# Kernel tuning notes

Hardware: AMD Instinct MI355X
Metric: run time of the kernel (lower is better)

The kernel has to match this reference:

```python
import jax, jax.numpy as jnp
import numpy as np

REG_WEIGHT = 1e-4
N_LAYERS = 3


def setup_inputs() -> dict:
    key = jax.random.key(0)
    ks = jax.random.split(key, 7)
    n_users, n_items, d = 100000, 50000, 64
    E, B = 1600000, 4096
    return {
        "user_table": jax.random.normal(ks[0], (n_users, d), dtype=jnp.float32) * 0.01,
        "item_table": jax.random.normal(ks[1], (n_items, d), dtype=jnp.float32) * 0.01,
        "edge_u": jax.random.randint(ks[2], (E,), 0, n_users, dtype=jnp.int32),
        "edge_i": jax.random.randint(ks[3], (E,), 0, n_items, dtype=jnp.int32),
        "users": jax.random.randint(ks[4], (B,), 0, n_users, dtype=jnp.int32),
        "pos_items": jax.random.randint(ks[5], (B,), 0, n_items, dtype=jnp.int32),
        "neg_items": jax.random.randint(ks[6], (B,), 0, n_items, dtype=jnp.int32),
    }


def _lightgcn_embeddings(user_table, item_table, edge_u, edge_i):
    n_users, n_items = user_table.shape[0], item_table.shape[0]
    N = n_users + n_items
    E = edge_u.shape[0]
    ones = jnp.ones((E,), dtype=user_table.dtype)
    # symmetric normalization D^{-1/2} A D^{-1/2} on the bipartite graph
    deg_u = jax.ops.segment_sum(ones, edge_u, num_segments=n_users)
    deg_i = jax.ops.segment_sum(ones, edge_i, num_segments=n_items)
    w = jax.lax.rsqrt(jnp.maximum(deg_u[edge_u] * deg_i[edge_i], 1.0))
    # symmetric edge list over the stacked [users; items] node set
    rows = jnp.concatenate([edge_u, edge_i + n_users])
    cols = jnp.concatenate([edge_i + n_users, edge_u])
    vals = jnp.concatenate([w, w])[:, None]

    x = jnp.concatenate([user_table, item_table], axis=0)  # [N, d]
    acc = x
    for _ in range(N_LAYERS):
        x = jax.ops.segment_sum(x[cols] * vals, rows, num_segments=N)
        acc = acc + x
    final = acc / jnp.asarray(N_LAYERS + 1, dtype=x.dtype)
    return final[:n_users], final[n_users:]


def reference(user_table, item_table, edge_u, edge_i, users, pos_items, neg_items):
    user_emb_all, item_emb_all = _lightgcn_embeddings(user_table, item_table, edge_u, edge_i)
    u_emb = user_emb_all[users]
    pos_i_emb = item_emb_all[pos_items]
    neg_i_emb = item_emb_all[neg_items]
    pos_scores = jnp.sum(u_emb * pos_i_emb, axis=-1)
    neg_scores = jnp.sum(u_emb * neg_i_emb, axis=-1)
    # L2 regularization on the layer-0 (table) embeddings
    u0 = user_table[users]
    p0 = item_table[pos_items]
    n0 = item_table[neg_items]
    reg_loss = REG_WEIGHT * (jnp.sum(u0 * u0) + jnp.sum(p0 * p0) + jnp.sum(n0 * n0))
    reg_loss = reg_loss / users.shape[0]
    return pos_scores, neg_scores, reg_loss
```

## Files before the change

### kernel.cpp

```cpp
#include <hip/hip_runtime.h>
#include <hip/hip_fp16.h>

#define THREADS 256
#define BIN_C2 4096
#define NBMAX 392
#define CAP 4608
#define SH_U 8
#define SH_I 7
#define CPAD 16
#define T_TILES 8
#define TSH_U 13
#define TSH_I 14

__global__ void binpack(const int* __restrict__ eu, const int* __restrict__ ei,
                        int* __restrict__ regu, int* __restrict__ regi,
                        int* __restrict__ sTu, int* __restrict__ sTi,
                        int E, int nbu, int nbi) {
    int c = blockIdx.x;
    bool isU = (blockIdx.y == 0);
    const int* key   = isU ? eu : ei;
    const int* other = isU ? ei : eu;
    int nb   = isU ? nbu : nbi;
    int sh   = isU ? SH_U : SH_I;
    int losh = isU ? 16 : 17;
    int lomsk = (1 << sh) - 1;
    int* reg = isU ? regu : regi;
    int* sT  = (isU ? sTu : sTi) + (size_t)c * (NBMAX);
    __shared__ int hist[NBMAX];
    __shared__ int wsum[4];
    int tid = threadIdx.x;
    int e0 = c * BIN_C2;
    int cnt = min(BIN_C2, E - e0);
    if (cnt <= 0) return;
    for (int b = tid; b < nb; b += THREADS) hist[b] = 0;
    __syncthreads();
    for (int k = tid; k < cnt; k += THREADS)
        atomicAdd(&hist[key[e0 + k] >> sh], 1);
    __syncthreads();
    int b0 = tid * 2;
    int v0 = (b0 < nb)     ? hist[b0]     : 0;
    int v1 = (b0 + 1 < nb) ? hist[b0 + 1] : 0;
    int s2 = v0 + v1;
    int lane = tid & 63, wid = tid >> 6;
    int inc = s2;
    #pragma unroll
    for (int ofs = 1; ofs < 64; ofs <<= 1) {
        int t = __shfl_up(inc, ofs);
        if (lane >= ofs) inc += t;
    }
    if (lane == 63) wsum[wid] = inc;
    __syncthreads();
    int wofs = 0;
    #pragma unroll
    for (int w = 0; w < 4; ++w) wofs += (w < wid) ? wsum[w] : 0;
    int excl = inc - s2 + wofs;
    __syncthreads();
    if (b0 < nb)     { hist[b0] = excl;          sT[b0] = excl; }
    if (b0 + 1 < nb) { hist[b0 + 1] = excl + v0; sT[b0 + 1] = excl + v0; }
    if (tid == THREADS - 1) sT[nb] = cnt;
    __syncthreads();
    for (int k = tid; k < cnt; k += THREADS) {
        int kn = key[e0 + k];
        int o  = other[e0 + k];
        int b  = kn >> sh;
        int p  = ((kn & lomsk) << losh) | o;
        int pos = atomicAdd(&hist[b], 1);
        reg[(size_t)c * BIN_C2 + pos] = p;
    }
}

__global__ void place(const int* __restrict__ regu, const int* __restrict__ regi,
                      const int* __restrict__ sTu, const int* __restrict__ sTi,
                      int* __restrict__ offu, int* __restrict__ offi,
                      int* __restrict__ du, int* __restrict__ di,
                      float* __restrict__ rsdu, float* __restrict__ rsdi,
                      int* __restrict__ entu, int* __restrict__ enti,
                      int* __restrict__ curs,
                      int nbu, int nU, int nI, int nchunks) {
    __shared__ int stash[CAP];
    __shared__ int bin_cnt[THREADS * T_TILES];
    __shared__ int node_base[THREADS];
    __shared__ int wsum[4];
    __shared__ int bob_sh;
    __shared__ int scursor;
    int b = blockIdx.x;
    bool isU = (b < nbu);
    int bidx = isU ? b : (b - nbu);
    const int* reg = isU ? regu : regi;
    const int* sT  = isU ? sTu : sTi;
    int base_node, nn;
    int *off, *deg, *ent; float* rsd;
    int losh, tsh;
    if (isU) {
        base_node = bidx << SH_U; nn = min(256, nU - base_node);
        off = offu; deg = du; rsd = rsdu; ent = entu;
        losh = 16; tsh = TSH_U;
    } else {
        base_node = bidx << SH_I; nn = min(128, nI - base_node);
        off = offi; deg = di; rsd = rsdi; ent = enti;
        losh = 17; tsh = TSH_I;
    }
    int lomask = (1 << losh) - 1;
    int tid = threadIdx.x;
    if (tid == 0) scursor = 0;
    #pragma unroll
    for (int t = 0; t < T_TILES; ++t) bin_cnt[tid + t * THREADS] = 0;
    __syncthreads();
    for (int c = tid; c < nchunks; c += THREADS) {
        const int* row = sT + (size_t)c * NBMAX;
        int s = row[bidx], e = row[bidx + 1];
        int len = e - s;
        if (len > 0) {
            int base = atomicAdd(&scursor, len);
            const int* src = reg + (size_t)c * BIN_C2 + s;
            for (int j = 0; j < len; ++j) {
                int pos = base + j;
                if (pos < CAP) stash[pos] = src[j];
            }
        }
    }
    __syncthreads();
    int count = min(scursor, CAP);
    for (int k = tid; k < count; k += THREADS) {
        int p = stash[k];
        int key = ((p >> losh) << 3) | ((p & lomask) >> tsh);
        atomicAdd(&bin_cnt[key], 1);
    }
    __syncthreads();
    int c = 0;
    {
        int base = tid * T_TILES;
        #pragma unroll
        for (int t = 0; t < T_TILES; ++t) {
            int v = bin_cnt[base + t];
            bin_cnt[base + t] = c;
            c += v;
        }
    }
    int seg = (c + 15) & ~15;
    int lane = tid & 63, wid = tid >> 6;
    int inc = seg;
    #pragma unroll
    for (int ofs = 1; ofs < 64; ofs <<= 1) {
        int t = __shfl_up(inc, ofs);
        if (lane >= ofs) inc += t;
    }
    if (lane == 63) wsum[wid] = inc;
    __syncthreads();
    int wofs = 0;
    #pragma unroll
    for (int w = 0; w < 4; ++w) wofs += (w < wid) ? wsum[w] : 0;
    int incl = inc + wofs;
    int excl = incl - seg;
    if (tid == THREADS - 1) bob_sh = atomicAdd(&curs[isU ? 0 : CPAD], incl);
    __syncthreads();
    int bob = bob_sh;
    node_base[tid] = excl;
    if (tid < nn) {
        off[base_node + tid] = bob + excl;
        deg[base_node + tid] = c;
        rsd[base_node + tid] = rsqrtf(fmaxf((float)c, 1.0f));
    }
    __syncthreads();
    #pragma unroll
    for (int t = 0; t < T_TILES; ++t) {
        int k = tid + t * THREADS;
        bin_cnt[k] += node_base[k >> 3];
    }
    __syncthreads();
    for (int k = tid; k < count; k += THREADS) {
        int p = stash[k];
        int key = ((p >> losh) << 3) | ((p & lomask) >> tsh);
        int sl = atomicAdd(&bin_cnt[key], 1);
        ent[bob + sl] = p & lomask;
    }
}

__global__ void conv16all(const float* __restrict__ ut, const float* __restrict__ it,
                          __half* __restrict__ dst, int nU16, int ntot16) {
    int stride = gridDim.x * blockDim.x;
    for (int i = blockIdx.x * blockDim.x + threadIdx.x; i < ntot16; i += stride) {
        const float* src = (i < nU16) ? (ut + (size_t)i * 4) : (it + (size_t)(i - nU16) * 4);
        float4 v = *reinterpret_cast<const float4*>(src);
        __half2 h0 = __float22half2_rn(make_float2(v.x, v.y));
        __half2 h1 = __float22half2_rn(make_float2(v.z, v.w));
        uint2 st;
        st.x = *reinterpret_cast<unsigned*>(&h0);
        st.y = *reinterpret_cast<unsigned*>(&h1);
        *reinterpret_cast<uint2*>(dst + (size_t)i * 4) = st;
    }
}

__global__ void prop16(const __half* __restrict__ x,
                       const int* __restrict__ offu, const int* __restrict__ offi,
                       const int* __restrict__ du, const int* __restrict__ di,
                       const float* __restrict__ rsdu, const float* __restrict__ rsdi,
                       const int* __restrict__ entu, const int* __restrict__ enti,
                       __half* __restrict__ y, int nU, int N) {
    int node = blockIdx.x * (THREADS >> 3) + (threadIdx.x >> 3);
    int lane = threadIdx.x & 7;
    if (node >= N) return;
    const int* ent; const __half* src; const float* rsdn;
    int beg, dg; float rs;
    if (node < nU) {
        beg = offu[node]; dg = du[node]; rs = rsdu[node];
        ent = entu; src = x + ((size_t)nU << 6); rsdn = rsdi;
    } else {
        int i = node - nU;
        beg = offi[i]; dg = di[i]; rs = rsdi[i];
        ent = enti; src = x; rsdn = rsdu;
    }
    float a0=0,a1=0,a2=0,a3=0,a4=0,a5=0,a6=0,a7=0;
    for (int k0 = 0; k0 < dg; k0 += 8) {
        int me = (k0 + lane < dg) ? ent[beg + k0 + lane] : 0;
        #pragma unroll
        for (int j = 0; j < 8; ++j) {
            if (k0 + j < dg) {
                int nbr = __shfl(me, j, 8);
                float w = rsdn[nbr];
                uint4 r = *reinterpret_cast<const uint4*>(src + ((size_t)nbr << 6) + (lane << 3));
                __half2 h0 = *reinterpret_cast<__half2*>(&r.x);
                __half2 h1 = *reinterpret_cast<__half2*>(&r.y);
                __half2 h2 = *reinterpret_cast<__half2*>(&r.z);
                __half2 h3 = *reinterpret_cast<__half2*>(&r.w);
                float2 f0 = __half22float2(h0), f1 = __half22float2(h1);
                float2 f2 = __half22float2(h2), f3 = __half22float2(h3);
                a0 += w * f0.x; a1 += w * f0.y; a2 += w * f1.x; a3 += w * f1.y;
                a4 += w * f2.x; a5 += w * f2.y; a6 += w * f3.x; a7 += w * f3.y;
            }
        }
    }
    __half2 o0 = __float22half2_rn(make_float2(a0 * rs, a1 * rs));
    __half2 o1 = __float22half2_rn(make_float2(a2 * rs, a3 * rs));
    __half2 o2 = __float22half2_rn(make_float2(a4 * rs, a5 * rs));
    __half2 o3 = __float22half2_rn(make_float2(a6 * rs, a7 * rs));
    uint4 st;
    st.x = *reinterpret_cast<unsigned*>(&o0);
    st.y = *reinterpret_cast<unsigned*>(&o1);
    st.z = *reinterpret_cast<unsigned*>(&o2);
    st.w = *reinterpret_cast<unsigned*>(&o3);
    *reinterpret_cast<uint4*>(y + ((size_t)node << 6) + (lane << 3)) = st;
}

__global__ void prop_sel_acc(const __half* __restrict__ x,
                             const int* __restrict__ users, const int* __restrict__ pos,
                             const int* __restrict__ neg,
                             const int* __restrict__ offu, const int* __restrict__ offi,
                             const int* __restrict__ du, const int* __restrict__ di,
                             const float* __restrict__ rsdu, const float* __restrict__ rsdi,
                             const int* __restrict__ entu, const int* __restrict__ enti,
                             float* __restrict__ sel, int B, int nU) {
    int r = blockIdx.x * (THREADS >> 3) + (threadIdx.x >> 3);
    int lane = threadIdx.x & 7;
    if (r >= 3 * B) return;
    int which = r / B, b = r - which * B;
    const int* ent; const __half* src; const float* rsdn;
    int beg, dg; float rs; size_t selfrow;
    if (which == 0) {
        int u = users[b];
        beg = offu[u]; dg = du[u]; rs = rsdu[u];
        ent = entu; src = x + ((size_t)nU << 6); rsdn = rsdi;
        selfrow = (size_t)u << 6;
    } else {
        int i = (which == 1) ? pos[b] : neg[b];
        beg = offi[i]; dg = di[i]; rs = rsdi[i];
        ent = enti; src = x; rsdn = rsdu;
        selfrow = (size_t)(nU + i) << 6;
    }
    float a0=0,a1=0,a2=0,a3=0,a4=0,a5=0,a6=0,a7=0;
    for (int k0 = 0; k0 < dg; k0 += 8) {
        int me = (k0 + lane < dg) ? ent[beg + k0 + lane] : 0;
        #pragma unroll
        for (int j = 0; j < 8; ++j) {
            if (k0 + j < dg) {
                int nbr = __shfl(me, j, 8);
                float w = rsdn[nbr];
                uint4 rv = *reinterpret_cast<const uint4*>(src + ((size_t)nbr << 6) + (lane << 3));
                __half2 h0 = *reinterpret_cast<__half2*>(&rv.x);
                __half2 h1 = *reinterpret_cast<__half2*>(&rv.y);
                __half2 h2 = *reinterpret_cast<__half2*>(&rv.z);
                __half2 h3 = *reinterpret_cast<__half2*>(&rv.w);
                float2 f0 = __half22float2(h0), f1 = __half22float2(h1);
                float2 f2 = __half22float2(h2), f3 = __half22float2(h3);
                a0 += w * f0.x; a1 += w * f0.y; a2 += w * f1.x; a3 += w * f1.y;
                a4 += w * f2.x; a5 += w * f2.y; a6 += w * f3.x; a7 += w * f3.y;
            }
        }
    }
    uint4 rv = *reinterpret_cast<const uint4*>(x + selfrow + (lane << 3));
    __half2 h0 = *reinterpret_cast<__half2*>(&rv.x);
    __half2 h1 = *reinterpret_cast<__half2*>(&rv.y);
    __half2 h2 = *reinterpret_cast<__half2*>(&rv.z);
    __half2 h3 = *reinterpret_cast<__half2*>(&rv.w);
    float2 s0 = __half22float2(h0), s1 = __half22float2(h1);
    float2 s2 = __half22float2(h2), s3 = __half22float2(h3);
    float* s = sel + ((size_t)r << 6) + (lane << 3);
    float4 d0 = *reinterpret_cast<float4*>(s);
    float4 d1 = *reinterpret_cast<float4*>(s + 4);
    d0.x += s0.x + rs * a0; d0.y += s0.y + rs * a1;
    d0.z += s1.x + rs * a2; d0.w += s1.y + rs * a3;
    d1.x += s2.x + rs * a4; d1.y += s2.y + rs * a5;
    d1.z += s3.x + rs * a6; d1.w += s3.y + rs * a7;
    *reinterpret_cast<float4*>(s) = d0;
    *reinterpret_cast<float4*>(s + 4) = d1;
}

__global__ void selreg(const float* __restrict__ ut, const float* __restrict__ it,
                       const int* __restrict__ users, const int* __restrict__ pos,
                       const int* __restrict__ neg,
                       float* __restrict__ sel, float* __restrict__ out_reg,
                       int B, float scale) {
    int r = blockIdx.x * (THREADS >> 4) + (threadIdx.x >> 4);
    int t = threadIdx.x & 15;
    float ssq = 0.f;
    if (r < 3 * B) {
        int which = r / B, b = r - which * B;
        const float* base; int idx;
        if (which == 0)      { base = ut; idx = users[b]; }
        else if (which == 1) { base = it; idx = pos[b]; }
        else                 { base = it; idx = neg[b]; }
        float4 v = *reinterpret_cast<const float4*>(base + ((size_t)idx << 6) + t * 4);
        *reinterpret_cast<float4*>(sel + ((size_t)r << 6) + t * 4) = v;
        ssq = v.x * v.x + v.y * v.y + v.z * v.z + v.w * v.w;
    }
    #pragma unroll
    for (int ofs = 32; ofs; ofs >>= 1) ssq += __shfl_down(ssq, ofs);
    if ((threadIdx.x & 63) == 0) atomicAdd(out_reg, ssq * scale);
}

__global__ void sel_acc16(const __half* __restrict__ x,
                          const int* __restrict__ users, const int* __restrict__ pos,
                          const int* __restrict__ neg, float* __restrict__ sel, int B, int nU) {
    int r = blockIdx.x * (THREADS >> 3) + (threadIdx.x >> 3);
    int lane = threadIdx.x & 7;
    if (r >= 3 * B) return;
    int which = r / B, b = r - which * B;
    size_t row;
    if (which == 0)      row = (size_t)users[b];
    else if (which == 1) row = (size_t)nU + pos[b];
    else                 row = (size_t)nU + neg[b];
    uint4 rv = *reinterpret_cast<const uint4*>(x + (row << 6) + (lane << 3));
    __half2 h0 = *reinterpret_cast<__half2*>(&rv.x);
    __half2 h1 = *reinterpret_cast<__half2*>(&rv.y);
    __half2 h2 = *reinterpret_cast<__half2*>(&rv.z);
    __half2 h3 = *reinterpret_cast<__half2*>(&rv.w);
    float2 f0 = __half22float2(h0), f1 = __half22float2(h1);
    float2 f2 = __half22float2(h2), f3 = __half22float2(h3);
    float* s = sel + ((size_t)r << 6) + (lane << 3);
    float4 d0 = *reinterpret_cast<float4*>(s);
    float4 d1 = *reinterpret_cast<float4*>(s + 4);
    d0.x += f0.x; d0.y += f0.y; d0.z += f1.x; d0.w += f1.y;
    d1.x += f2.x; d1.y += f2.y; d1.z += f3.x; d1.w += f3.y;
    *reinterpret_cast<float4*>(s) = d0;
    *reinterpret_cast<float4*>(s + 4) = d1;
}

__global__ void score(const float* __restrict__ sel, float* __restrict__ out, int B) {
    int b = blockIdx.x * (THREADS >> 6) + (threadIdx.x >> 6);
    int lane = threadIdx.x & 63;
    if (b >= B) return;
    float u = sel[((size_t)b << 6) + lane];
    float p = sel[((size_t)(B + b) << 6) + lane];
    float n = sel[((size_t)(2 * B + b) << 6) + lane];
    float ps = u * p, ns = u * n;
    for (int ofs = 32; ofs; ofs >>= 1) {
        ps += __shfl_down(ps, ofs);
        ns += __shfl_down(ns, ofs);
    }
    if (lane == 0) {
        out[b]     = ps * (1.0f / 16.0f);
        out[B + b] = ns * (1.0f / 16.0f);
    }
}

extern "C" void kernel_launch(void* const* d_in, const int* in_sizes, int n_in,
                              void* d_out, int out_size, void* d_ws, size_t ws_size,
                              hipStream_t stream) {
    const float* ut   = (const float*)d_in[0];
    const float* it   = (const float*)d_in[1];
    const int* eu     = (const int*)d_in[2];
    const int* ei     = (const int*)d_in[3];
    const int* users  = (const int*)d_in[4];
    const int* pos    = (const int*)d_in[5];
    const int* neg    = (const int*)d_in[6];
    int nU = in_sizes[0] / 64;
    int nI = in_sizes[1] / 64;
    int E  = in_sizes[2];
    int B  = in_sizes[4];
    int N  = nU + nI;
    float* out = (float*)d_out;

    int nbu = (nU + 255) >> SH_U;
    int nbi = (nI + 127) >> SH_I;
    int nchunks = (E + BIN_C2 - 1) / BIN_C2;

    char* ws = (char*)d_ws;
    size_t cursor = 0;
    auto alloc = [&](size_t bytes) -> void* {
        cursor = (cursor + 255) & ~(size_t)255;
        void* p = ws + cursor;
        cursor += bytes;
        return p;
    };
    int*   curs = (int*)alloc(2 * CPAD * 4);
    size_t zero_span = cursor;
    int*   regu = (int*)alloc((size_t)nchunks * BIN_C2 * 4);
    int*   regi = (int*)alloc((size_t)nchunks * BIN_C2 * 4);
    int*   sTu  = (int*)alloc((size_t)nchunks * NBMAX * 4);
    int*   sTi  = (int*)alloc((size_t)nchunks * NBMAX * 4);
    int*   offu = (int*)alloc((size_t)nU * 4);
    int*   offi = (int*)alloc((size_t)nI * 4);
    int*   du   = (int*)alloc((size_t)nU * 4);
    int*   di   = (int*)alloc((size_t)nI * 4);
    float* rsdu = (float*)alloc((size_t)nU * 4);
    float* rsdi = (float*)alloc((size_t)nI * 4);
    int*   entu = (int*)alloc(((size_t)E + (size_t)nbu * 256 * 16) * 4);
    int*   enti = (int*)alloc(((size_t)E + (size_t)nbi * 128 * 16) * 4);
    __half* xA  = (__half*)alloc((size_t)N * 64 * 2);
    __half* xB  = (__half*)alloc((size_t)N * 64 * 2);
    float* sel  = (float*)alloc((size_t)3 * B * 64 * 4);

    hipMemsetAsync(d_ws, 0, zero_span, stream);
    hipMemsetAsync(out + 2 * B, 0, sizeof(float), stream);

    conv16all<<<2048, THREADS, 0, stream>>>(ut, it, xA, nU * 16, N * 16);

    binpack<<<dim3(nchunks, 2), THREADS, 0, stream>>>(eu, ei, regu, regi, sTu, sTi, E, nbu, nbi);
    place<<<nbu + nbi, THREADS, 0, stream>>>(regu, regi, sTu, sTi,
                                             offu, offi, du, di, rsdu, rsdi, entu, enti,
                                             curs, nbu, nU, nI, nchunks);

    selreg<<<(3 * B + 15) / 16, THREADS, 0, stream>>>(ut, it, users, pos, neg, sel,
                                                      out + 2 * B, B, 1e-4f / (float)B);

    int gridSel16 = (3 * B * 8 + THREADS - 1) / THREADS;
    int gridProp = (N * 8 + THREADS - 1) / THREADS;
    prop16<<<gridProp, THREADS, 0, stream>>>(xA, offu, offi, du, di, rsdu, rsdi, entu, enti, xB, nU, N);
    sel_acc16<<<gridSel16, THREADS, 0, stream>>>(xB, users, pos, neg, sel, B, nU);
    prop16<<<gridProp, THREADS, 0, stream>>>(xB, offu, offi, du, di, rsdu, rsdi, entu, enti, xA, nU, N);
    prop_sel_acc<<<gridSel16, THREADS, 0, stream>>>(xA, users, pos, neg, offu, offi, du, di,
                                                    rsdu, rsdi, entu, enti, sel, B, nU);

    score<<<(B + 3) / 4, THREADS, 0, stream>>>(sel, out, B);
}
```

Before: 280.6 us.

## Merge independent kernels into shared launches and use nontemporal loads/stores in propagation

Three pairs of independent kernels now share one launch each, with block ranges split between the two jobs: the fp32-to-fp16 table conversion runs alongside binpack, selreg alongside place, and sel_acc16 alongside the second propagation layer. This cuts launch count and lets independent work overlap on the GPU instead of running one after another. Edge index loads and the propagated-row stores now use nontemporal builtins to reduce cache pollution. The cost is heterogeneous blocks within a single grid, possible load imbalance, and nontemporal stores on data that the next layer reads again.

```diff
diff --git a/kernel.cpp b/kernel.cpp
--- a/kernel.cpp
+++ b/kernel.cpp
@@ -12,12 +12,31 @@
 #define TSH_U 13
 #define TSH_I 14
 
-__global__ void binpack(const int* __restrict__ eu, const int* __restrict__ ei,
-                        int* __restrict__ regu, int* __restrict__ regi,
-                        int* __restrict__ sTu, int* __restrict__ sTi,
-                        int E, int nbu, int nbi) {
+typedef unsigned u32x4 __attribute__((ext_vector_type(4)));
+
+__global__ void build_conv(const float* __restrict__ ut, const float* __restrict__ it,
+                           __half* __restrict__ dst, int nU16, int ntot16,
+                           const int* __restrict__ eu, const int* __restrict__ ei,
+                           int* __restrict__ regu, int* __restrict__ regi,
+                           int* __restrict__ sTu, int* __restrict__ sTi,
+                           int E, int nbu, int nbi, int nchunks) {
+    if (blockIdx.y == 0) {
+        int stride = gridDim.x * blockDim.x;
+        for (int i = blockIdx.x * blockDim.x + threadIdx.x; i < ntot16; i += stride) {
+            const float* src = (i < nU16) ? (ut + (size_t)i * 4) : (it + (size_t)(i - nU16) * 4);
+            float4 v = *reinterpret_cast<const float4*>(src);
+            __half2 h0 = __float22half2_rn(make_float2(v.x, v.y));
+            __half2 h1 = __float22half2_rn(make_float2(v.z, v.w));
+            uint2 st;
+            st.x = *reinterpret_cast<unsigned*>(&h0);
+            st.y = *reinterpret_cast<unsigned*>(&h1);
+            *reinterpret_cast<uint2*>(dst + (size_t)i * 4) = st;
+        }
+        return;
+    }
     int c = blockIdx.x;
-    bool isU = (blockIdx.y == 0);
+    if (c >= nchunks) return;
+    bool isU = (blockIdx.y == 1);
     const int* key   = isU ? eu : ei;
     const int* other = isU ? ei : eu;
     int nb   = isU ? nbu : nbi;
@@ -25,7 +44,7 @@
     int losh = isU ? 16 : 17;
     int lomsk = (1 << sh) - 1;
     int* reg = isU ? regu : regi;
-    int* sT  = (isU ? sTu : sTi) + (size_t)c * (NBMAX);
+    int* sT  = (isU ? sTu : sTi) + (size_t)c * NBMAX;
     __shared__ int hist[NBMAX];
     __shared__ int wsum[4];
     int tid = threadIdx.x;
@@ -69,14 +88,40 @@
     }
 }
 
-__global__ void place(const int* __restrict__ regu, const int* __restrict__ regi,
-                      const int* __restrict__ sTu, const int* __restrict__ sTi,
-                      int* __restrict__ offu, int* __restrict__ offi,
-                      int* __restrict__ du, int* __restrict__ di,
-                      float* __restrict__ rsdu, float* __restrict__ rsdi,
-                      int* __restrict__ entu, int* __restrict__ enti,
-                      int* __restrict__ curs,
-                      int nbu, int nU, int nI, int nchunks) {
+__global__ void place_selreg(const int* __restrict__ regu, const int* __restrict__ regi,
+                             const int* __restrict__ sTu, const int* __restrict__ sTi,
+                             int* __restrict__ offu, int* __restrict__ offi,
+                             int* __restrict__ du, int* __restrict__ di,
+                             float* __restrict__ rsdu, float* __restrict__ rsdi,
+                             int* __restrict__ entu, int* __restrict__ enti,
+                             int* __restrict__ curs,
+                             int nbu, int nbi, int nU, int nI, int nchunks,
+                             const float* __restrict__ ut, const float* __restrict__ it,
+                             const int* __restrict__ users, const int* __restrict__ pos,
+                             const int* __restrict__ neg,
+                             float* __restrict__ sel, float* __restrict__ out_reg,
+                             int B, float scale) {
+    int nbTot = nbu + nbi;
+    int tid = threadIdx.x;
+    if (blockIdx.x >= nbTot) {
+        int r = (blockIdx.x - nbTot) * (THREADS >> 4) + (tid >> 4);
+        int t = tid & 15;
+        float ssq = 0.f;
+        if (r < 3 * B) {
+            int which = r / B, b = r - which * B;
+            const float* base; int idx;
+            if (which == 0)      { base = ut; idx = users[b]; }
+            else if (which == 1) { base = it; idx = pos[b]; }
+            else                 { base = it; idx = neg[b]; }
+            float4 v = *reinterpret_cast<const float4*>(base + ((size_t)idx << 6) + t * 4);
+            *reinterpret_cast<float4*>(sel + ((size_t)r << 6) + t * 4) = v;
+            ssq = v.x * v.x + v.y * v.y + v.z * v.z + v.w * v.w;
+        }
+        #pragma unroll
+        for (int ofs = 32; ofs; ofs >>= 1) ssq += __shfl_down(ssq, ofs);
+        if ((tid & 63) == 0) atomicAdd(out_reg, ssq * scale);
+        return;
+    }
     __shared__ int stash[CAP];
     __shared__ int bin_cnt[THREADS * T_TILES];
     __shared__ int node_base[THREADS];
@@ -101,7 +146,6 @@
         losh = 17; tsh = TSH_I;
     }
     int lomask = (1 << losh) - 1;
-    int tid = threadIdx.x;
     if (tid == 0) scursor = 0;
     #pragma unroll
     for (int t = 0; t < T_TILES; ++t) bin_cnt[tid + t * THREADS] = 0;
@@ -114,8 +158,8 @@
             int base = atomicAdd(&scursor, len);
             const int* src = reg + (size_t)c * BIN_C2 + s;
             for (int j = 0; j < len; ++j) {
-                int pos = base + j;
-                if (pos < CAP) stash[pos] = src[j];
+                int p = base + j;
+                if (p < CAP) stash[p] = src[j];
             }
         }
     }
@@ -176,29 +220,12 @@
     }
 }
 
-__global__ void conv16all(const float* __restrict__ ut, const float* __restrict__ it,
-                          __half* __restrict__ dst, int nU16, int ntot16) {
-    int stride = gridDim.x * blockDim.x;
-    for (int i = blockIdx.x * blockDim.x + threadIdx.x; i < ntot16; i += stride) {
-        const float* src = (i < nU16) ? (ut + (size_t)i * 4) : (it + (size_t)(i - nU16) * 4);
-        float4 v = *reinterpret_cast<const float4*>(src);
-        __half2 h0 = __float22half2_rn(make_float2(v.x, v.y));
-        __half2 h1 = __float22half2_rn(make_float2(v.z, v.w));
-        uint2 st;
-        st.x = *reinterpret_cast<unsigned*>(&h0);
-        st.y = *reinterpret_cast<unsigned*>(&h1);
-        *reinterpret_cast<uint2*>(dst + (size_t)i * 4) = st;
-    }
-}
-
-__global__ void prop16(const __half* __restrict__ x,
-                       const int* __restrict__ offu, const int* __restrict__ offi,
-                       const int* __restrict__ du, const int* __restrict__ di,
-                       const float* __restrict__ rsdu, const float* __restrict__ rsdi,
-                       const int* __restrict__ entu, const int* __restrict__ enti,
-                       __half* __restrict__ y, int nU, int N) {
-    int node = blockIdx.x * (THREADS >> 3) + (threadIdx.x >> 3);
-    int lane = threadIdx.x & 7;
+__device__ __forceinline__ void prop_body(const __half* __restrict__ x,
+                                          const int* __restrict__ offu, const int* __restrict__ offi,
+                                          const int* __restrict__ du, const int* __restrict__ di,
+                                          const float* __restrict__ rsdu, const float* __restrict__ rsdi,
+                                          const int* __restrict__ entu, const int* __restrict__ enti,
+                                          __half* __restrict__ y, int nU, int N, int node, int lane) {
     if (node >= N) return;
     const int* ent; const __half* src; const float* rsdn;
     int beg, dg; float rs;
@@ -212,7 +239,7 @@
     }
     float a0=0,a1=0,a2=0,a3=0,a4=0,a5=0,a6=0,a7=0;
     for (int k0 = 0; k0 < dg; k0 += 8) {
-        int me = (k0 + lane < dg) ? ent[beg + k0 + lane] : 0;
+        int me = (k0 + lane < dg) ? __builtin_nontemporal_load(&ent[beg + k0 + lane]) : 0;
         #pragma unroll
         for (int j = 0; j < 8; ++j) {
             if (k0 + j < dg) {
@@ -234,12 +261,59 @@
     __half2 o1 = __float22half2_rn(make_float2(a2 * rs, a3 * rs));
     __half2 o2 = __float22half2_rn(make_float2(a4 * rs, a5 * rs));
     __half2 o3 = __float22half2_rn(make_float2(a6 * rs, a7 * rs));
-    uint4 st;
+    u32x4 st;
     st.x = *reinterpret_cast<unsigned*>(&o0);
     st.y = *reinterpret_cast<unsigned*>(&o1);
     st.z = *reinterpret_cast<unsigned*>(&o2);
     st.w = *reinterpret_cast<unsigned*>(&o3);
-    *reinterpret_cast<uint4*>(y + ((size_t)node << 6) + (lane << 3)) = st;
+    __builtin_nontemporal_store(st, reinterpret_cast<u32x4*>(y + ((size_t)node << 6) + (lane << 3)));
+}
+
+__global__ void prop16(const __half* __restrict__ x,
+                       const int* __restrict__ offu, const int* __restrict__ offi,
+                       const int* __restrict__ du, const int* __restrict__ di,
+                       const float* __restrict__ rsdu, const float* __restrict__ rsdi,
+                       const int* __restrict__ entu, const int* __restrict__ enti,
+                       __half* __restrict__ y, int nU, int N) {
+    int node = blockIdx.x * (THREADS >> 3) + (threadIdx.x >> 3);
+    prop_body(x, offu, offi, du, di, rsdu, rsdi, entu, enti, y, nU, N, node, threadIdx.x & 7);
+}
+
+__global__ void prop16_selacc(const __half* __restrict__ x,
+                              const int* __restrict__ offu, const int* __restrict__ offi,
+                              const int* __restrict__ du, const int* __restrict__ di,
+                              const float* __restrict__ rsdu, const float* __restrict__ rsdi,
+                              const int* __restrict__ entu, const int* __restrict__ enti,
+                              __half* __restrict__ y, int nU, int N, int gridProp,
+                              const int* __restrict__ users, const int* __restrict__ pos,
+                              const int* __restrict__ neg, float* __restrict__ sel, int B) {
+    int lane = threadIdx.x & 7;
+    if (blockIdx.x < gridProp) {
+        int node = blockIdx.x * (THREADS >> 3) + (threadIdx.x >> 3);
+        prop_body(x, offu, offi, du, di, rsdu, rsdi, entu, enti, y, nU, N, node, lane);
+        return;
+    }
+    int r = (blockIdx.x - gridProp) * (THREADS >> 3) + (threadIdx.x >> 3);
+    if (r >= 3 * B) return;
+    int which = r / B, b = r - which * B;
+    size_t row;
+    if (which == 0)      row = (size_t)users[b];
+    else if (which == 1) row = (size_t)nU + pos[b];
+    else                 row = (size_t)nU + neg[b];
+    uint4 rv = *reinterpret_cast<const uint4*>(x + (row << 6) + (lane << 3));
+    __half2 h0 = *reinterpret_cast<__half2*>(&rv.x);
+    __half2 h1 = *reinterpret_cast<__half2*>(&rv.y);
+    __half2 h2 = *reinterpret_cast<__half2*>(&rv.z);
+    __half2 h3 = *reinterpret_cast<__half2*>(&rv.w);
+    float2 f0 = __half22float2(h0), f1 = __half22float2(h1);
+    float2 f2 = __half22float2(h2), f3 = __half22float2(h3);
+    float* s = sel + ((size_t)r << 6) + (lane << 3);
+    float4 d0 = *reinterpret_cast<float4*>(s);
+    float4 d1 = *reinterpret_cast<float4*>(s + 4);
+    d0.x += f0.x; d0.y += f0.y; d0.z += f1.x; d0.w += f1.y;
+    d1.x += f2.x; d1.y += f2.y; d1.z += f3.x; d1.w += f3.y;
+    *reinterpret_cast<float4*>(s) = d0;
+    *reinterpret_cast<float4*>(s + 4) = d1;
 }
 
 __global__ void prop_sel_acc(const __half* __restrict__ x,
@@ -269,7 +343,7 @@
     }
     float a0=0,a1=0,a2=0,a3=0,a4=0,a5=0,a6=0,a7=0;
     for (int k0 = 0; k0 < dg; k0 += 8) {
-        int me = (k0 + lane < dg) ? ent[beg + k0 + lane] : 0;
+        int me = (k0 + lane < dg) ? __builtin_nontemporal_load(&ent[beg + k0 + lane]) : 0;
         #pragma unroll
         for (int j = 0; j < 8; ++j) {
             if (k0 + j < dg) {
@@ -301,56 +375,6 @@
     d0.z += s1.x + rs * a2; d0.w += s1.y + rs * a3;
     d1.x += s2.x + rs * a4; d1.y += s2.y + rs * a5;
     d1.z += s3.x + rs * a6; d1.w += s3.y + rs * a7;
-    *reinterpret_cast<float4*>(s) = d0;
-    *reinterpret_cast<float4*>(s + 4) = d1;
-}
-
-__global__ void selreg(const float* __restrict__ ut, const float* __restrict__ it,
-                       const int* __restrict__ users, const int* __restrict__ pos,
-                       const int* __restrict__ neg,
-                       float* __restrict__ sel, float* __restrict__ out_reg,
-                       int B, float scale) {
-    int r = blockIdx.x * (THREADS >> 4) + (threadIdx.x >> 4);
-    int t = threadIdx.x & 15;
-    float ssq = 0.f;
-    if (r < 3 * B) {
-        int which = r / B, b = r - which * B;
-        const float* base; int idx;
-        if (which == 0)      { base = ut; idx = users[b]; }
-        else if (which == 1) { base = it; idx = pos[b]; }
-        else                 { base = it; idx = neg[b]; }
-        float4 v = *reinterpret_cast<const float4*>(base + ((size_t)idx << 6) + t * 4);
-        *reinterpret_cast<float4*>(sel + ((size_t)r << 6) + t * 4) = v;
-        ssq = v.x * v.x + v.y * v.y + v.z * v.z + v.w * v.w;
-    }
-    #pragma unroll
-    for (int ofs = 32; ofs; ofs >>= 1) ssq += __shfl_down(ssq, ofs);
-    if ((threadIdx.x & 63) == 0) atomicAdd(out_reg, ssq * scale);
-}
-
-__global__ void sel_acc16(const __half* __restrict__ x,
-                          const int* __restrict__ users, const int* __restrict__ pos,
-                          const int* __restrict__ neg, float* __restrict__ sel, int B, int nU) {
-    int r = blockIdx.x * (THREADS >> 3) + (threadIdx.x >> 3);
-    int lane = threadIdx.x & 7;
-    if (r >= 3 * B) return;
-    int which = r / B, b = r - which * B;
-    size_t row;
-    if (which == 0)      row = (size_t)users[b];
-    else if (which == 1) row = (size_t)nU + pos[b];
-    else                 row = (size_t)nU + neg[b];
-    uint4 rv = *reinterpret_cast<const uint4*>(x + (row << 6) + (lane << 3));
-    __half2 h0 = *reinterpret_cast<__half2*>(&rv.x);
-    __half2 h1 = *reinterpret_cast<__half2*>(&rv.y);
-    __half2 h2 = *reinterpret_cast<__half2*>(&rv.z);
-    __half2 h3 = *reinterpret_cast<__half2*>(&rv.w);
-    float2 f0 = __half22float2(h0), f1 = __half22float2(h1);
-    float2 f2 = __half22float2(h2), f3 = __half22float2(h3);
-    float* s = sel + ((size_t)r << 6) + (lane << 3);
-    float4 d0 = *reinterpret_cast<float4*>(s);
-    float4 d1 = *reinterpret_cast<float4*>(s + 4);
-    d0.x += f0.x; d0.y += f0.y; d0.z += f1.x; d0.w += f1.y;
-    d1.x += f2.x; d1.y += f2.y; d1.z += f3.x; d1.w += f3.y;
     *reinterpret_cast<float4*>(s) = d0;
     *reinterpret_cast<float4*>(s + 4) = d1;
 }
@@ -423,21 +447,25 @@
     hipMemsetAsync(d_ws, 0, zero_span, stream);
     hipMemsetAsync(out + 2 * B, 0, sizeof(float), stream);
 
-    conv16all<<<2048, THREADS, 0, stream>>>(ut, it, xA, nU * 16, N * 16);
-
-    binpack<<<dim3(nchunks, 2), THREADS, 0, stream>>>(eu, ei, regu, regi, sTu, sTi, E, nbu, nbi);
-    place<<<nbu + nbi, THREADS, 0, stream>>>(regu, regi, sTu, sTi,
-                                             offu, offi, du, di, rsdu, rsdi, entu, enti,
-                                             curs, nbu, nU, nI, nchunks);
-
-    selreg<<<(3 * B + 15) / 16, THREADS, 0, stream>>>(ut, it, users, pos, neg, sel,
-                                                      out + 2 * B, B, 1e-4f / (float)B);
+    int gbx = max(nchunks, 1024);
+    build_conv<<<dim3(gbx, 3), THREADS, 0, stream>>>(ut, it, xA, nU * 16, N * 16,
+                                                     eu, ei, regu, regi, sTu, sTi,
+                                                     E, nbu, nbi, nchunks);
+
+    int selregBlocks = (3 * B + 15) / 16;
+    place_selreg<<<nbu + nbi + selregBlocks, THREADS, 0, stream>>>(
+        regu, regi, sTu, sTi, offu, offi, du, di, rsdu, rsdi, entu, enti,
+        curs, nbu, nbi, nU, nI, nchunks,
+        ut, it, users, pos, neg, sel, out + 2 * B, B, 1e-4f / (float)B);
 
     int gridSel16 = (3 * B * 8 + THREADS - 1) / THREADS;
     int gridProp = (N * 8 + THREADS - 1) / THREADS;
     prop16<<<gridProp, THREADS, 0, stream>>>(xA, offu, offi, du, di, rsdu, rsdi, entu, enti, xB, nU, N);
-    sel_acc16<<<gridSel16, THREADS, 0, stream>>>(xB, users, pos, neg, sel, B, nU);
-    prop16<<<gridProp, THREADS, 0, stream>>>(xB, offu, offi, du, di, rsdu, rsdi, entu, enti, xA, nU, N);
+
+    prop16_selacc<<<gridProp + gridSel16, THREADS, 0, stream>>>(
+        xB, offu, offi, du, di, rsdu, rsdi, entu, enti, xA, nU, N, gridProp,
+        users, pos, neg, sel, B);
+
     prop_sel_acc<<<gridSel16, THREADS, 0, stream>>>(xA, users, pos, neg, offu, offi, du, di,
                                                     rsdu, rsdi, entu, enti, sel, B, nU);
 
```

New measurement: 282.0 us. Within noise of the previous version (+0.5%).
